# Optimization experiments

Hardware: AMD Instinct MI355X
Metric: run time of the kernel (lower is better)

## Reference

```python
import jax, jax.numpy as jnp
import numpy as np

IN_DIM, HID, MEM, OUT = 512, 1024, 1024, 512
BATCH = 4096
HIST = 5  # hist_steps hard-coded in MMU.__init__

_LINEARS = [("inpgate", IN_DIM, HID), ("rec_inpgate", OUT, HID), ("mem_inpgate", MEM, HID),
            ("inp", IN_DIM, HID), ("rec_inp", OUT, HID),
            ("readgate", IN_DIM, MEM), ("rec_readgate", OUT, MEM), ("mem_readgate", MEM, MEM),
            ("decoder", HID, MEM),
            ("writegate", IN_DIM, MEM), ("rec_writegate", OUT, MEM), ("mem_writegate", MEM, MEM),
            ("encoder", MEM, HID)]


def setup_inputs() -> dict:
    key = jax.random.key(0)
    ks = iter(jax.random.split(key, 2 * len(_LINEARS) + 4))
    d = {"input": jax.random.normal(next(ks), (IN_DIM, BATCH), jnp.float32)}
    for name, fin, fout in _LINEARS:
        bound = 1.0 / np.sqrt(fin)  # torch nn.Linear default init range
        d["W_" + name] = jax.random.uniform(next(ks), (fout, fin), jnp.float32, -bound, bound)
        d["b_" + name] = jax.random.uniform(next(ks), (fout,), jnp.float32, -bound, bound)
    d["w_hid_out"] = jax.random.uniform(next(ks), (OUT, MEM), jnp.float32)  # torch.rand
    return d


def reference(input, W_inpgate, b_inpgate, W_rec_inpgate, b_rec_inpgate,
              W_mem_inpgate, b_mem_inpgate, W_inp, b_inp, W_rec_inp, b_rec_inp,
              W_readgate, b_readgate, W_rec_readgate, b_rec_readgate,
              W_mem_readgate, b_mem_readgate, W_decoder, b_decoder,
              W_writegate, b_writegate, W_rec_writegate, b_rec_writegate,
              W_mem_writegate, b_mem_writegate, W_encoder, b_encoder, w_hid_out):
    B = input.shape[1]
    lin = lambda x, W, b: x @ W.T + b
    # fresh module: history is zeros except last slot = current input (transposed to [B, in])
    xs = jnp.concatenate([jnp.zeros((HIST - 1, B, IN_DIM), input.dtype), input.T[None]], axis=0)

    def step(carry, x):
        out, mem = carry  # [B, OUT], [B, MEM]
        block_inp = jax.nn.sigmoid(lin(x, W_inp, b_inp) + lin(out, W_rec_inp, b_rec_inp))
        inp_gate = jax.nn.sigmoid(lin(x, W_inpgate, b_inpgate) + lin(mem, W_mem_inpgate, b_mem_inpgate)
                                  + lin(out, W_rec_inpgate, b_rec_inpgate))
        read_gate = jax.nn.sigmoid(lin(x, W_readgate, b_readgate) + lin(mem, W_mem_readgate, b_mem_readgate)
                                   + lin(out, W_rec_readgate, b_rec_readgate))
        decoded_mem = lin(read_gate * mem, W_decoder, b_decoder)
        hidden = decoded_mem + block_inp * inp_gate  # [B, HID] (HID == MEM)
        write_gate = jax.nn.sigmoid(lin(x, W_writegate, b_writegate) + lin(mem, W_mem_writegate, b_mem_writegate)
                                    + lin(out, W_rec_writegate, b_rec_writegate))
        encoded = jnp.tanh(lin(hidden, W_encoder, b_encoder))
        mem = (1.0 - write_gate) * mem + write_gate * encoded
        out = hidden @ w_hid_out.T  # w_hid_out.mm(hidden.T).T
        return (out, mem), None

    init = (jnp.zeros((B, OUT), input.dtype), jnp.zeros((B, MEM), input.dtype))
    (out, _mem), _ = jax.lax.scan(step, init, xs)
    return out
```

## Files before the change

kernel.cpp:

```cpp
#include <hip/hip_runtime.h>
#include <hip/hip_bf16.h>
#include <math.h>

typedef __hip_bfloat16 bf16;
typedef __attribute__((ext_vector_type(8))) short s16x8;
typedef __attribute__((ext_vector_type(4))) float f32x4;

__device__ __forceinline__ float fsig(float x) {
  return __builtin_amdgcn_rcpf(1.0f + __expf(-x));
}
__device__ __forceinline__ float ftanh(float x) { return 2.0f * fsig(2.0f * x) - 1.0f; }
__device__ __forceinline__ float dot4(float4 a, float4 b) {
  return a.x * b.x + a.y * b.y + a.z * b.z + a.w * b.w;
}
__device__ __forceinline__ float wred(float s) {
#pragma unroll
  for (int off = 32; off > 0; off >>= 1) s += __shfl_down(s, off, 64);
  return s;
}

__global__ void setup(const float* __restrict__ W_inp, const float* __restrict__ W_ig,
                      const float* __restrict__ W_rg, const float* __restrict__ W_ho,
                      const float* __restrict__ W_dec, const float* __restrict__ W_enc,
                      const float* __restrict__ input,
                      const float* __restrict__ b_inp, const float* __restrict__ b_rinp,
                      const float* __restrict__ b_ig, const float* __restrict__ b_mig,
                      const float* __restrict__ b_rig, const float* __restrict__ b_wg,
                      const float* __restrict__ b_mwg, const float* __restrict__ b_rwg,
                      const float* __restrict__ b_dec, const float* __restrict__ b_enc,
                      bf16* __restrict__ Wcat,
                      bf16* __restrict__ WhoB, bf16* __restrict__ Wcat2, bf16* __restrict__ Wdt,
                      bf16* __restrict__ WencB, bf16* __restrict__ Xb,
                      float* __restrict__ out_s, float* __restrict__ mem_s,
                      float* __restrict__ vout, float* __restrict__ Web) {
  __shared__ float t[32][33];
  const int id = blockIdx.x, tid = threadIdx.x;
  if (id < 12288) {
    const int i = id * 256 + tid;
    if (i < 524288) {
      Wcat[i] = __float2bfloat16(W_inp[i]);
    } else if (i < 1048576) {
      Wcat[i] = __float2bfloat16(W_ig[i - 524288]);
    } else if (i < 1572864) {
      Wcat[i] = __float2bfloat16(W_rg[i - 1048576]);
    } else if (i < 2097152) {
      const int k = i - 1572864;
      const bf16 vv = __float2bfloat16(W_ho[k]);
      WhoB[k] = vv;
      Wcat2[(size_t)(k >> 10) * 2048 + (k & 1023)] = vv;
    } else {
      const int k = i - 2097152;
      WencB[k] = __float2bfloat16(W_enc[k]);
    }
  } else if (id < 14336) {
    const int b = id - 12288;
    const int i0 = (b >> 7) * 32, b0 = (b & 127) * 32;
    const int tx = tid & 31, ty = tid >> 5;
#pragma unroll
    for (int r = ty; r < 32; r += 8) t[r][tx] = input[(size_t)(i0 + r) * 4096 + b0 + tx];
    __syncthreads();
#pragma unroll
    for (int r = ty; r < 32; r += 8)
      Xb[(size_t)(b0 + r) * 512 + i0 + tx] = __float2bfloat16(t[tx][r]);
  } else if (id < 15360) {
    const int b = id - 14336;
    const int j0 = (b >> 5) * 32, k0 = (b & 31) * 32;
    const int tx = tid & 31, ty = tid >> 5;
#pragma unroll
    for (int r = ty; r < 32; r += 8) t[r][tx] = W_dec[(size_t)(j0 + r) * 1024 + k0 + tx];
    __syncthreads();
#pragma unroll
    for (int r = ty; r < 32; r += 8)
      Wdt[(size_t)(k0 + r) * 1024 + j0 + tx] = __float2bfloat16(t[tx][r]);
  } else if (id < 16896) {
    const int o = id - 15360;
    const float* row = (o < 512) ? (W_ho + (size_t)o * 1024) : (W_enc + (size_t)(o - 512) * 1024);
    const float4 a = *(const float4*)(row + tid * 4);
    const float4 b = *(const float4*)(b_dec + tid * 4);
    float s = wred(dot4(a, b));
    if ((tid & 63) == 0) t[0][tid >> 6] = s;
    __syncthreads();
    if (tid == 0) {
      const float d = t[0][0] + t[0][1] + t[0][2] + t[0][3];
      if (o < 512) vout[o] = d;
      else Web[o - 512] = d;
    }
  } else {
    const int id2 = id - 16896;
    const float4 bd = *(const float4*)(b_dec + tid * 4);
    const float4 v1 = *(const float4*)(b_inp + tid * 4);
    const float4 v2 = *(const float4*)(b_rinp + tid * 4);
    const float4 v3 = *(const float4*)(b_ig + tid * 4);
    const float4 v4 = *(const float4*)(b_mig + tid * 4);
    const float4 v5 = *(const float4*)(b_rig + tid * 4);
    float4 hv;
    hv.x = bd.x + fsig(v1.x + v2.x) * fsig(v3.x + v4.x + v5.x);
    hv.y = bd.y + fsig(v1.y + v2.y) * fsig(v3.y + v4.y + v5.y);
    hv.z = bd.z + fsig(v1.z + v2.z) * fsig(v3.z + v4.z + v5.z);
    hv.w = bd.w + fsig(v1.w + v2.w) * fsig(v3.w + v4.w + v5.w);
    const float* row =
        (id2 < 1024) ? (W_enc + (size_t)id2 * 1024) : (W_ho + (size_t)(id2 - 1024) * 1024);
    float s = wred(dot4(*(const float4*)(row + tid * 4), hv));
    if ((tid & 63) == 0) t[0][tid >> 6] = s;
    __syncthreads();
    if (tid == 0) {
      const float d = t[0][0] + t[0][1] + t[0][2] + t[0][3];
      if (id2 < 1024) {
        const float wg = fsig(b_wg[id2] + b_mwg[id2] + b_rwg[id2]);
        mem_s[id2] = wg * ftanh(b_enc[id2] + d);
      } else {
        out_s[id2 - 1024] = d;
      }
    }
  }
}

__global__ __launch_bounds__(256) void gates_pe(
    const float* __restrict__ Wri, const float* __restrict__ Wmig,
    const float* __restrict__ Wrig, const float* __restrict__ Wmrg,
    const float* __restrict__ Wrrg, const float* __restrict__ Wmwg,
    const float* __restrict__ Wrwg, const float* __restrict__ b_inp,
    const float* __restrict__ b_rinp, const float* __restrict__ b_ig,
    const float* __restrict__ b_mig, const float* __restrict__ b_rig,
    const float* __restrict__ b_rg, const float* __restrict__ b_mrg,
    const float* __restrict__ b_rrg, const float* __restrict__ b_wg,
    const float* __restrict__ b_mwg, const float* __restrict__ b_rwg,
    const float* __restrict__ out_s, const float* __restrict__ mem_s,
    float* __restrict__ rgm, float* __restrict__ h0v, float* __restrict__ wgv,
    const bf16* __restrict__ WhoB, const bf16* __restrict__ WencB,
    const bf16* __restrict__ Wdt, float* __restrict__ P, float* __restrict__ E,
    int pe_blocks) {
  __shared__ char smem[16384];
  const int tid = threadIdx.x;
  if ((int)blockIdx.x >= pe_blocks) {
    float(*red)[4] = (float(*)[4])smem;
    const int j = blockIdx.x - pe_blocks, lane = tid & 63, wave = tid >> 6;
    const float4 z = make_float4(0.f, 0.f, 0.f, 0.f);
    const float4 o4 = (tid < 128) ? *(const float4*)(out_s + tid * 4) : z;
    const float4 m4 = *(const float4*)(mem_s + tid * 4);
    float p[7];
    p[0] = dot4((tid < 128) ? *(const float4*)(Wri + (size_t)j * 512 + tid * 4) : z, o4);
    p[1] = dot4(*(const float4*)(Wmig + (size_t)j * 1024 + tid * 4), m4);
    p[2] = dot4((tid < 128) ? *(const float4*)(Wrig + (size_t)j * 512 + tid * 4) : z, o4);
    p[3] = dot4(*(const float4*)(Wmrg + (size_t)j * 1024 + tid * 4), m4);
    p[4] = dot4((tid < 128) ? *(const float4*)(Wrrg + (size_t)j * 512 + tid * 4) : z, o4);
    p[5] = dot4(*(const float4*)(Wmwg + (size_t)j * 1024 + tid * 4), m4);
    p[6] = dot4((tid < 128) ? *(const float4*)(Wrwg + (size_t)j * 512 + tid * 4) : z, o4);
#pragma unroll
    for (int d = 0; d < 7; ++d) {
      float s = wred(p[d]);
      if (lane == 0) red[d][wave] = s;
    }
    __syncthreads();
    if (tid == 0) {
      float D[7];
#pragma unroll
      for (int d = 0; d < 7; ++d) D[d] = red[d][0] + red[d][1] + red[d][2] + red[d][3];
      const float abi = b_inp[j] + b_rinp[j] + D[0];
      const float aig = b_ig[j] + b_mig[j] + b_rig[j] + D[1] + D[2];
      const float arg = b_rg[j] + b_mrg[j] + b_rrg[j] + D[3] + D[4];
      const float awg = b_wg[j] + b_mwg[j] + b_rwg[j] + D[5] + D[6];
      rgm[j] = fsig(arg) * mem_s[j];
      h0v[j] = fsig(abi) * fsig(aig);
      wgv[j] = fsig(awg);
    }
    return;
  }
  const int bi = blockIdx.x;
  const bf16* Ag;
  float* Cg;
  int m0, n0, kt0;
  if (bi < 256) {
    Ag = WhoB; Cg = P;
    m0 = ((bi >> 4) & 7) * 64; n0 = (bi & 15) * 64; kt0 = (bi >> 7) * 512;
  } else {
    const int b2 = bi - 256;
    Ag = WencB; Cg = E;
    m0 = ((b2 >> 4) & 15) * 64; n0 = (b2 & 15) * 64; kt0 = (b2 >> 8) * 512;
  }
  const int wave = tid >> 6, lane = tid & 63;
  const int wm = wave >> 1, wn = wave & 1;
  f32x4 acc[2][2] = {};
  for (int kt = kt0; kt < kt0 + 512; kt += 64) {
    __syncthreads();
#pragma unroll
    for (int i = 0; i < 2; ++i) {
      const int ci = i * 256 + tid;
      const int row = ci >> 3, ck = (ci & 7) ^ (row & 7);
      const bf16* g = Ag + (size_t)(m0 + row) * 1024 + kt + ck * 8;
      const unsigned lofs = (unsigned)__builtin_amdgcn_readfirstlane((i * 256 + wave * 64) * 16);
      __builtin_amdgcn_global_load_lds(
          (const __attribute__((address_space(1))) void*)g,
          (__attribute__((address_space(3))) void*)(smem + lofs), 16, 0, 0);
    }
#pragma unroll
    for (int i = 0; i < 2; ++i) {
      const int ci = i * 256 + tid;
      const int row = ci >> 3, ck = (ci & 7) ^ (row & 7);
      const bf16* g = Wdt + (size_t)(n0 + row) * 1024 + kt + ck * 8;
      const unsigned lofs =
          (unsigned)__builtin_amdgcn_readfirstlane(8192 + (i * 256 + wave * 64) * 16);
      __builtin_amdgcn_global_load_lds(
          (const __attribute__((address_space(1))) void*)g,
          (__attribute__((address_space(3))) void*)(smem + lofs), 16, 0, 0);
    }
    __syncthreads();
#pragma unroll
    for (int ks = 0; ks < 2; ++ks) {
      const int ckk = ks * 4 + (lane >> 4);
      s16x8 af[2];
#pragma unroll
      for (int i = 0; i < 2; ++i) {
        const int R = wm * 32 + i * 16 + (lane & 15);
        af[i] = *(const s16x8*)(smem + (R * 8 + (ckk ^ (R & 7))) * 16);
      }
#pragma unroll
      for (int j = 0; j < 2; ++j) {
        const int R = wn * 32 + j * 16 + (lane & 15);
        const s16x8 bfr = *(const s16x8*)(smem + 8192 + (R * 8 + (ckk ^ (R & 7))) * 16);
#pragma unroll
        for (int i = 0; i < 2; ++i)
          acc[i][j] = __builtin_amdgcn_mfma_f32_16x16x32_bf16(af[i], bfr, acc[i][j], 0, 0, 0);
      }
    }
  }
  const int mb = (lane >> 4) * 4, nb = lane & 15;
#pragma unroll
  for (int i = 0; i < 2; ++i) {
#pragma unroll
    for (int j = 0; j < 2; ++j) {
      const int col = n0 + wn * 32 + j * 16 + nb;
#pragma unroll
      for (int r = 0; r < 4; ++r) {
        const int rowg = m0 + wm * 32 + i * 16 + mb + r;
        atomicAdd(Cg + (size_t)rowg * 1024 + col, acc[i][j][r]);
      }
    }
  }
}

__global__ void step_fuse(const float* __restrict__ E, const float* __restrict__ Wenc,
                          const float* __restrict__ P, const float* __restrict__ Who,
                          const float* __restrict__ b_enc, const float* __restrict__ Web,
                          const float* __restrict__ vout, const float* __restrict__ rgm,
                          const float* __restrict__ h0v, const float* __restrict__ wgv,
                          float* __restrict__ mem_s, float* __restrict__ out_s) {
  __shared__ float red[4];
  const int id = blockIdx.x, tid = threadIdx.x;
  const float4 r4 = *(const float4*)(rgm + tid * 4);
  const float4 h4 = *(const float4*)(h0v + tid * 4);
  const float* Ar = (id < 1024) ? (E + (size_t)id * 1024) : (P + (size_t)(id - 1024) * 1024);
  const float* Br = (id < 1024) ? (Wenc + (size_t)id * 1024) : (Who + (size_t)(id - 1024) * 1024);
  const float s1 = dot4(*(const float4*)(Ar + tid * 4), r4);
  const float s2 = dot4(*(const float4*)(Br + tid * 4), h4);
  const float s = wred(s1 + s2);
  if ((tid & 63) == 0) red[tid >> 6] = s;
  __syncthreads();
  if (tid == 0) {
    const float d = red[0] + red[1] + red[2] + red[3];
    if (id < 1024) {
      const float wg = wgv[id];
      mem_s[id] = (1.0f - wg) * mem_s[id] + wg * ftanh(b_enc[id] + Web[id] + d);
    } else {
      out_s[id - 1024] = vout[id - 1024] + d;
    }
  }
}

__global__ void final_consts(const float* __restrict__ Wri, const float* __restrict__ Wmig,
                             const float* __restrict__ Wrig, const float* __restrict__ Wmrg,
                             const float* __restrict__ Wrrg, const float* __restrict__ b_inp,
                             const float* __restrict__ b_rinp, const float* __restrict__ b_ig,
                             const float* __restrict__ b_mig, const float* __restrict__ b_rig,
                             const float* __restrict__ b_rg, const float* __restrict__ b_mrg,
                             const float* __restrict__ b_rrg, const float* __restrict__ out_s,
                             const float* __restrict__ mem_s, const float* __restrict__ P,
                             float* __restrict__ ccat, bf16* __restrict__ Wcat2) {
  __shared__ float red[5][4];
  const int id = blockIdx.x, tid = threadIdx.x, lane = tid & 63, wave = tid >> 6;
  if (id < 1024) {
    const float4 z = make_float4(0.f, 0.f, 0.f, 0.f);
    const float4 o4 = (tid < 128) ? *(const float4*)(out_s + tid * 4) : z;
    const float4 m4 = *(const float4*)(mem_s + tid * 4);
    float p[5];
    p[0] = dot4((tid < 128) ? *(const float4*)(Wri + (size_t)id * 512 + tid * 4) : z, o4);
    p[1] = dot4(*(const float4*)(Wmig + (size_t)id * 1024 + tid * 4), m4);
    p[2] = dot4((tid < 128) ? *(const float4*)(Wrig + (size_t)id * 512 + tid * 4) : z, o4);
    p[3] = dot4(*(const float4*)(Wmrg + (size_t)id * 1024 + tid * 4), m4);
    p[4] = dot4((tid < 128) ? *(const float4*)(Wrrg + (size_t)id * 512 + tid * 4) : z, o4);
#pragma unroll
    for (int d = 0; d < 5; ++d) {
      float s = wred(p[d]);
      if (lane == 0) red[d][wave] = s;
    }
    __syncthreads();
    if (tid == 0) {
      float D[5];
#pragma unroll
      for (int d = 0; d < 5; ++d) D[d] = red[d][0] + red[d][1] + red[d][2] + red[d][3];
      ccat[id] = b_inp[id] + b_rinp[id] + D[0];
      ccat[1024 + id] = b_ig[id] + b_mig[id] + b_rig[id] + D[1] + D[2];
      ccat[2048 + id] = b_rg[id] + b_mrg[id] + b_rrg[id] + D[3] + D[4];
    }
  } else {
    const int idx = (id - 1024) * 256 + tid;
    const int q = idx >> 10, k = idx & 1023;
    Wcat2[(size_t)q * 2048 + 1024 + k] = __float2bfloat16(P[idx] * mem_s[k]);
  }
}

__global__ __launch_bounds__(256, 4) void gemm_gates(const bf16* __restrict__ A,
                                                     const bf16* __restrict__ Wcat,
                                                     const float* __restrict__ ccat,
                                                     bf16* __restrict__ Hcat) {
  __shared__ char smem[32768];
  const int tid = threadIdx.x, wave = tid >> 6, lane = tid & 63;
  const int wm = wave >> 1, wn = wave & 1;
  const int m0 = blockIdx.y * 64, n0 = blockIdx.x * 64;
  f32x4 acc[3][2][2] = {};

  for (int kt = 0; kt < 512; kt += 64) {
    __syncthreads();
#pragma unroll
    for (int i = 0; i < 2; ++i) {
      const int ci = i * 256 + tid;
      const int row = ci >> 3, ck = (ci & 7) ^ (row & 7);
      const bf16* g = A + (size_t)(m0 + row) * 512 + kt + ck * 8;
      const unsigned lofs = (unsigned)__builtin_amdgcn_readfirstlane((i * 256 + wave * 64) * 16);
      __builtin_amdgcn_global_load_lds(
          (const __attribute__((address_space(1))) void*)g,
          (__attribute__((address_space(3))) void*)(smem + lofs), 16, 0, 0);
    }
#pragma unroll
    for (int gI = 0; gI < 3; ++gI) {
      const bf16* Bp = Wcat + gI * 524288;
#pragma unroll
      for (int i = 0; i < 2; ++i) {
        const int ci = i * 256 + tid;
        const int row = ci >> 3, ck = (ci & 7) ^ (row & 7);
        const bf16* g = Bp + (size_t)(n0 + row) * 512 + kt + ck * 8;
        const unsigned lofs = (unsigned)__builtin_amdgcn_readfirstlane(
            8192 + gI * 8192 + (i * 256 + wave * 64) * 16);
        __builtin_amdgcn_global_load_lds(
            (const __attribute__((address_space(1))) void*)g,
            (__attribute__((address_space(3))) void*)(smem + lofs), 16, 0, 0);
      }
    }
    __syncthreads();

#pragma unroll
    for (int ks = 0; ks < 2; ++ks) {
      const int ckk = ks * 4 + (lane >> 4);
      s16x8 af[2];
#pragma unroll
      for (int i = 0; i < 2; ++i) {
        const int R = wm * 32 + i * 16 + (lane & 15);
        af[i] = *(const s16x8*)(smem + (R * 8 + (ckk ^ (R & 7))) * 16);
      }
#pragma unroll
      for (int gI = 0; gI < 3; ++gI) {
#pragma unroll
        for (int j = 0; j < 2; ++j) {
          const int R = wn * 32 + j * 16 + (lane & 15);
          const s16x8 bfr =
              *(const s16x8*)(smem + 8192 + gI * 8192 + (R * 8 + (ckk ^ (R & 7))) * 16);
#pragma unroll
          for (int i = 0; i < 2; ++i)
            acc[gI][i][j] =
                __builtin_amdgcn_mfma_f32_16x16x32_bf16(af[i], bfr, acc[gI][i][j], 0, 0, 0);
        }
      }
    }
  }

  __syncthreads();
  bf16* sm = (bf16*)smem;
  bf16* sr = (bf16*)smem + 5120;
  const int mb = (lane >> 4) * 4, nb = lane & 15;
#pragma unroll
  for (int i = 0; i < 2; ++i) {
#pragma unroll
    for (int j = 0; j < 2; ++j) {
      const int colL = wn * 32 + j * 16 + nb;
      const int jg = n0 + colL;
      const float c0 = ccat[jg], c1 = ccat[1024 + jg], c2 = ccat[2048 + jg];
#pragma unroll
      for (int r = 0; r < 4; ++r) {
        const int rowL = wm * 32 + i * 16 + mb + r;
        const float h = fsig(acc[0][i][j][r] + c0) * fsig(acc[1][i][j][r] + c1);
        const float rg = fsig(acc[2][i][j][r] + c2);
        sm[rowL * 80 + colL] = __float2bfloat16(h);
        sr[rowL * 80 + colL] = __float2bfloat16(rg);
      }
    }
  }
  __syncthreads();
#pragma unroll
  for (int pp = 0; pp < 2; ++pp) {
    const int c = pp * 256 + tid;
    const int row = c >> 3, cc = c & 7;
    const s16x8 v0 = *(const s16x8*)(sm + row * 80 + cc * 8);
    const s16x8 v1 = *(const s16x8*)(sr + row * 80 + cc * 8);
    *(s16x8*)(Hcat + (size_t)(m0 + row) * 2048 + n0 + cc * 8) = v0;
    *(s16x8*)(Hcat + (size_t)(m0 + row) * 2048 + 1024 + n0 + cc * 8) = v1;
  }
}

__global__ __launch_bounds__(256, 4) void gemm_out(const bf16* __restrict__ A,
                                                   const bf16* __restrict__ Bp,
                                                   const float* __restrict__ vout,
                                                   float* __restrict__ outF) {
  __shared__ char smem[16384];
  const int tid = threadIdx.x, wave = tid >> 6, lane = tid & 63;
  const int wm = wave >> 1, wn = wave & 1;
  const int m0 = blockIdx.y * 64, n0 = blockIdx.x * 64;
  f32x4 acc[2][2] = {};

  for (int kt = 0; kt < 2048; kt += 64) {
    __syncthreads();
#pragma unroll
    for (int i = 0; i < 2; ++i) {
      const int ci = i * 256 + tid;
      const int row = ci >> 3, ck = (ci & 7) ^ (row & 7);
      const bf16* g = A + (size_t)(m0 + row) * 2048 + kt + ck * 8;
      const unsigned lofs = (unsigned)__builtin_amdgcn_readfirstlane((i * 256 + wave * 64) * 16);
      __builtin_amdgcn_global_load_lds(
          (const __attribute__((address_space(1))) void*)g,
          (__attribute__((address_space(3))) void*)(smem + lofs), 16, 0, 0);
    }
#pragma unroll
    for (int i = 0; i < 2; ++i) {
      const int ci = i * 256 + tid;
      const int row = ci >> 3, ck = (ci & 7) ^ (row & 7);
      const bf16* g = Bp + (size_t)(n0 + row) * 2048 + kt + ck * 8;
      const unsigned lofs =
          (unsigned)__builtin_amdgcn_readfirstlane(8192 + (i * 256 + wave * 64) * 16);
      __builtin_amdgcn_global_load_lds(
          (const __attribute__((address_space(1))) void*)g,
          (__attribute__((address_space(3))) void*)(smem + lofs), 16, 0, 0);
    }
    __syncthreads();

#pragma unroll
    for (int ks = 0; ks < 2; ++ks) {
      const int ckk = ks * 4 + (lane >> 4);
      s16x8 af[2];
#pragma unroll
      for (int i = 0; i < 2; ++i) {
        const int R = wm * 32 + i * 16 + (lane & 15);
        af[i] = *(const s16x8*)(smem + (R * 8 + (ckk ^ (R & 7))) * 16);
      }
#pragma unroll
      for (int j = 0; j < 2; ++j) {
        const int R = wn * 32 + j * 16 + (lane & 15);
        const s16x8 bfr = *(const s16x8*)(smem + 8192 + (R * 8 + (ckk ^ (R & 7))) * 16);
#pragma unroll
        for (int i = 0; i < 2; ++i)
          acc[i][j] = __builtin_amdgcn_mfma_f32_16x16x32_bf16(af[i], bfr, acc[i][j], 0, 0, 0);
      }
    }
  }

  const int mb = (lane >> 4) * 4, nb = lane & 15;
#pragma unroll
  for (int i = 0; i < 2; ++i) {
#pragma unroll
    for (int j = 0; j < 2; ++j) {
      const int col = n0 + wn * 32 + j * 16 + nb;
#pragma unroll
      for (int r = 0; r < 4; ++r) {
        const int rowg = m0 + wm * 32 + i * 16 + mb + r;
        outF[(size_t)rowg * 512 + col] = acc[i][j][r] + vout[col];
      }
    }
  }
}

extern "C" void kernel_launch(void* const* d_in, const int* in_sizes, int n_in, void* d_out,
                              int out_size, void* d_ws, size_t ws_size, hipStream_t stream) {
  const float* input  = (const float*)d_in[0];
  const float* W_ig   = (const float*)d_in[1];  const float* b_ig   = (const float*)d_in[2];
  const float* W_rig  = (const float*)d_in[3];  const float* b_rig  = (const float*)d_in[4];
  const float* W_mig  = (const float*)d_in[5];  const float* b_mig  = (const float*)d_in[6];
  const float* W_inp  = (const float*)d_in[7];  const float* b_inp  = (const float*)d_in[8];
  const float* W_rinp = (const float*)d_in[9];  const float* b_rinp = (const float*)d_in[10];
  const float* W_rg   = (const float*)d_in[11]; const float* b_rg   = (const float*)d_in[12];
  const float* W_rrg  = (const float*)d_in[13]; const float* b_rrg  = (const float*)d_in[14];
  const float* W_mrg  = (const float*)d_in[15]; const float* b_mrg  = (const float*)d_in[16];
  const float* W_dec  = (const float*)d_in[17]; const float* b_dec  = (const float*)d_in[18];
  const float* W_wg   = (const float*)d_in[19]; const float* b_wg   = (const float*)d_in[20];
  const float* W_rwg  = (const float*)d_in[21]; const float* b_rwg  = (const float*)d_in[22];
  const float* W_mwg  = (const float*)d_in[23]; const float* b_mwg  = (const float*)d_in[24];
  const float* W_enc  = (const float*)d_in[25]; const float* b_enc  = (const float*)d_in[26];
  const float* W_ho   = (const float*)d_in[27];
  (void)W_wg;

  char* ws = (char*)d_ws;
  float* out_s = (float*)(ws + 0);
  float* mem_s = (float*)(ws + 4096);
  float* rgm   = (float*)(ws + 8192);
  float* h0v   = (float*)(ws + 12288);
  float* wgv   = (float*)(ws + 16384);
  float* ccat  = (float*)(ws + 24576);
  float* vout  = (float*)(ws + 40960);
  float* Web   = (float*)(ws + 45056);
  float* P     = (float*)(ws + 65536);
  bf16* Xb     = (bf16*)(ws + 2162688);
  bf16* Wcat   = (bf16*)(ws + 6356992);
  bf16* WhoB   = (bf16*)(ws + 9502720);
  bf16* Wcat2  = (bf16*)(ws + 10551296);
  bf16* Wdt    = (bf16*)(ws + 12648448);
  bf16* Hcat   = (bf16*)(ws + 14745600);
  float* E     = (float*)(ws + 31522816);
  bf16* WencB  = (bf16*)(ws + 35717120);

  setup<<<18432, 256, 0, stream>>>(W_inp, W_ig, W_rg, W_ho, W_dec, W_enc, input, b_inp, b_rinp,
                                   b_ig, b_mig, b_rig, b_wg, b_mwg, b_rwg, b_dec, b_enc, Wcat,
                                   WhoB, Wcat2, Wdt, WencB, Xb, out_s, mem_s, vout, Web);

  for (int s = 0; s < 3; ++s) {
    const int pe = (s == 0) ? 768 : 0;
    gates_pe<<<1024 + pe, 256, 0, stream>>>(W_rinp, W_mig, W_rig, W_mrg, W_rrg, W_mwg, W_rwg,
                                            b_inp, b_rinp, b_ig, b_mig, b_rig, b_rg, b_mrg,
                                            b_rrg, b_wg, b_mwg, b_rwg, out_s, mem_s, rgm, h0v,
                                            wgv, WhoB, WencB, Wdt, P, E, pe);
    step_fuse<<<1536, 256, 0, stream>>>(E, W_enc, P, W_ho, b_enc, Web, vout, rgm, h0v, wgv,
                                        mem_s, out_s);
  }

  final_consts<<<3072, 256, 0, stream>>>(W_rinp, W_mig, W_rig, W_mrg, W_rrg, b_inp, b_rinp, b_ig,
                                         b_mig, b_rig, b_rg, b_mrg, b_rrg, out_s, mem_s, P, ccat,
                                         Wcat2);

  gemm_gates<<<dim3(16, 64), 256, 0, stream>>>(Xb, Wcat, ccat, Hcat);

  gemm_out<<<dim3(8, 64), 256, 0, stream>>>(Hcat, Wcat2, vout, (float*)d_out);
}
```

Before: 227.7 us.

## Double-buffer GEMM LDS staging, drop split-K atomics, store P/E products in bf16

The precompute GEMM in gates_pe no longer splits K in two with fp32 atomicAdd. Each block now runs the full K=1024 and writes bf16 results directly, so there are half as many blocks. Both that GEMM and gemm_out now double-buffer their LDS tiles (32 KB), prefetching the next k-slice while MFMAs run on the current one. step_fuse and final_consts read the bf16 P/E products and the bf16 weight copies instead of fp32, which halves their read traffic. The costs are less parallelism in the step-0 GEMM, twice the shared memory per block (which may lower occupancy), and extra rounding error from bf16 intermediates.

```diff
diff --git a/kernel.cpp b/kernel.cpp
--- a/kernel.cpp
+++ b/kernel.cpp
@@ -17,6 +17,12 @@
 #pragma unroll
   for (int off = 32; off > 0; off >>= 1) s += __shfl_down(s, off, 64);
   return s;
+}
+__device__ __forceinline__ float b2f(unsigned short u) {
+  return __uint_as_float((unsigned)u << 16);
+}
+__device__ __forceinline__ float4 b2f4(ushort4 u) {
+  return make_float4(b2f(u.x), b2f(u.y), b2f(u.z), b2f(u.w));
 }
 
 __global__ void setup(const float* __restrict__ W_inp, const float* __restrict__ W_ig,
@@ -128,9 +134,9 @@
     const float* __restrict__ out_s, const float* __restrict__ mem_s,
     float* __restrict__ rgm, float* __restrict__ h0v, float* __restrict__ wgv,
     const bf16* __restrict__ WhoB, const bf16* __restrict__ WencB,
-    const bf16* __restrict__ Wdt, float* __restrict__ P, float* __restrict__ E,
+    const bf16* __restrict__ Wdt, bf16* __restrict__ Pb, bf16* __restrict__ Eb,
     int pe_blocks) {
-  __shared__ char smem[16384];
+  __shared__ char smem[32768];
   const int tid = threadIdx.x;
   if ((int)blockIdx.x >= pe_blocks) {
     float(*red)[4] = (float(*)[4])smem;
@@ -168,27 +174,28 @@
   }
   const int bi = blockIdx.x;
   const bf16* Ag;
-  float* Cg;
-  int m0, n0, kt0;
-  if (bi < 256) {
-    Ag = WhoB; Cg = P;
-    m0 = ((bi >> 4) & 7) * 64; n0 = (bi & 15) * 64; kt0 = (bi >> 7) * 512;
+  bf16* Cg;
+  int m0, n0;
+  if (bi < 128) {
+    Ag = WhoB; Cg = Pb;
+    m0 = (bi >> 4) * 64; n0 = (bi & 15) * 64;
   } else {
-    const int b2 = bi - 256;
-    Ag = WencB; Cg = E;
-    m0 = ((b2 >> 4) & 15) * 64; n0 = (b2 & 15) * 64; kt0 = (b2 >> 8) * 512;
+    const int b2 = bi - 128;
+    Ag = WencB; Cg = Eb;
+    m0 = (b2 >> 4) * 64; n0 = (b2 & 15) * 64;
   }
   const int wave = tid >> 6, lane = tid & 63;
   const int wm = wave >> 1, wn = wave & 1;
   f32x4 acc[2][2] = {};
-  for (int kt = kt0; kt < kt0 + 512; kt += 64) {
-    __syncthreads();
+
+  auto STAGE = [&](int kt, unsigned bofs) {
 #pragma unroll
     for (int i = 0; i < 2; ++i) {
       const int ci = i * 256 + tid;
       const int row = ci >> 3, ck = (ci & 7) ^ (row & 7);
       const bf16* g = Ag + (size_t)(m0 + row) * 1024 + kt + ck * 8;
-      const unsigned lofs = (unsigned)__builtin_amdgcn_readfirstlane((i * 256 + wave * 64) * 16);
+      const unsigned lofs =
+          (unsigned)__builtin_amdgcn_readfirstlane(bofs + (i * 256 + wave * 64) * 16);
       __builtin_amdgcn_global_load_lds(
           (const __attribute__((address_space(1))) void*)g,
           (__attribute__((address_space(3))) void*)(smem + lofs), 16, 0, 0);
@@ -199,30 +206,39 @@
       const int row = ci >> 3, ck = (ci & 7) ^ (row & 7);
       const bf16* g = Wdt + (size_t)(n0 + row) * 1024 + kt + ck * 8;
       const unsigned lofs =
-          (unsigned)__builtin_amdgcn_readfirstlane(8192 + (i * 256 + wave * 64) * 16);
+          (unsigned)__builtin_amdgcn_readfirstlane(bofs + 8192 + (i * 256 + wave * 64) * 16);
       __builtin_amdgcn_global_load_lds(
           (const __attribute__((address_space(1))) void*)g,
           (__attribute__((address_space(3))) void*)(smem + lofs), 16, 0, 0);
     }
-    __syncthreads();
+  };
+
+  STAGE(0, 0);
+  __syncthreads();
+  unsigned cur = 0;
+  for (int kt = 0; kt < 1024; kt += 64) {
+    if (kt + 64 < 1024) STAGE(kt + 64, (cur ^ 1u) * 16384u);
 #pragma unroll
     for (int ks = 0; ks < 2; ++ks) {
       const int ckk = ks * 4 + (lane >> 4);
+      const unsigned cofs = cur * 16384u;
       s16x8 af[2];
 #pragma unroll
       for (int i = 0; i < 2; ++i) {
         const int R = wm * 32 + i * 16 + (lane & 15);
-        af[i] = *(const s16x8*)(smem + (R * 8 + (ckk ^ (R & 7))) * 16);
+        af[i] = *(const s16x8*)(smem + cofs + (R * 8 + (ckk ^ (R & 7))) * 16);
       }
 #pragma unroll
       for (int j = 0; j < 2; ++j) {
         const int R = wn * 32 + j * 16 + (lane & 15);
-        const s16x8 bfr = *(const s16x8*)(smem + 8192 + (R * 8 + (ckk ^ (R & 7))) * 16);
+        const s16x8 bfr = *(const s16x8*)(smem + cofs + 8192 + (R * 8 + (ckk ^ (R & 7))) * 16);
 #pragma unroll
         for (int i = 0; i < 2; ++i)
           acc[i][j] = __builtin_amdgcn_mfma_f32_16x16x32_bf16(af[i], bfr, acc[i][j], 0, 0, 0);
       }
     }
+    __syncthreads();
+    cur ^= 1u;
   }
   const int mb = (lane >> 4) * 4, nb = lane & 15;
 #pragma unroll
@@ -233,14 +249,14 @@
 #pragma unroll
       for (int r = 0; r < 4; ++r) {
         const int rowg = m0 + wm * 32 + i * 16 + mb + r;
-        atomicAdd(Cg + (size_t)rowg * 1024 + col, acc[i][j][r]);
-      }
-    }
-  }
-}
-
-__global__ void step_fuse(const float* __restrict__ E, const float* __restrict__ Wenc,
-                          const float* __restrict__ P, const float* __restrict__ Who,
+        Cg[(size_t)rowg * 1024 + col] = __float2bfloat16(acc[i][j][r]);
+      }
+    }
+  }
+}
+
+__global__ void step_fuse(const bf16* __restrict__ Eb, const bf16* __restrict__ WencB,
+                          const bf16* __restrict__ Pb, const bf16* __restrict__ WhoB,
                           const float* __restrict__ b_enc, const float* __restrict__ Web,
                           const float* __restrict__ vout, const float* __restrict__ rgm,
                           const float* __restrict__ h0v, const float* __restrict__ wgv,
@@ -249,11 +265,12 @@
   const int id = blockIdx.x, tid = threadIdx.x;
   const float4 r4 = *(const float4*)(rgm + tid * 4);
   const float4 h4 = *(const float4*)(h0v + tid * 4);
-  const float* Ar = (id < 1024) ? (E + (size_t)id * 1024) : (P + (size_t)(id - 1024) * 1024);
-  const float* Br = (id < 1024) ? (Wenc + (size_t)id * 1024) : (Who + (size_t)(id - 1024) * 1024);
-  const float s1 = dot4(*(const float4*)(Ar + tid * 4), r4);
-  const float s2 = dot4(*(const float4*)(Br + tid * 4), h4);
-  const float s = wred(s1 + s2);
+  const bf16* Ar = (id < 1024) ? (Eb + (size_t)id * 1024) : (Pb + (size_t)(id - 1024) * 1024);
+  const bf16* Br =
+      (id < 1024) ? (WencB + (size_t)id * 1024) : (WhoB + (size_t)(id - 1024) * 1024);
+  const float4 a4 = b2f4(*(const ushort4*)(Ar + tid * 4));
+  const float4 b4 = b2f4(*(const ushort4*)(Br + tid * 4));
+  const float s = wred(dot4(a4, r4) + dot4(b4, h4));
   if ((tid & 63) == 0) red[tid >> 6] = s;
   __syncthreads();
   if (tid == 0) {
@@ -274,7 +291,7 @@
                              const float* __restrict__ b_mig, const float* __restrict__ b_rig,
                              const float* __restrict__ b_rg, const float* __restrict__ b_mrg,
                              const float* __restrict__ b_rrg, const float* __restrict__ out_s,
-                             const float* __restrict__ mem_s, const float* __restrict__ P,
+                             const float* __restrict__ mem_s, const bf16* __restrict__ Pb,
                              float* __restrict__ ccat, bf16* __restrict__ Wcat2) {
   __shared__ float red[5][4];
   const int id = blockIdx.x, tid = threadIdx.x, lane = tid & 63, wave = tid >> 6;
@@ -304,8 +321,9 @@
     }
   } else {
     const int idx = (id - 1024) * 256 + tid;
-    const int q = idx >> 10, k = idx & 1023;
-    Wcat2[(size_t)q * 2048 + 1024 + k] = __float2bfloat16(P[idx] * mem_s[k]);
+    const int k = idx & 1023;
+    const float pv = b2f(((const unsigned short*)Pb)[idx]);
+    Wcat2[(size_t)(idx >> 10) * 2048 + 1024 + k] = __float2bfloat16(pv * mem_s[k]);
   }
 }
 
@@ -410,20 +428,20 @@
                                                    const bf16* __restrict__ Bp,
                                                    const float* __restrict__ vout,
                                                    float* __restrict__ outF) {
-  __shared__ char smem[16384];
+  __shared__ char smem[32768];
   const int tid = threadIdx.x, wave = tid >> 6, lane = tid & 63;
   const int wm = wave >> 1, wn = wave & 1;
   const int m0 = blockIdx.y * 64, n0 = blockIdx.x * 64;
   f32x4 acc[2][2] = {};
 
-  for (int kt = 0; kt < 2048; kt += 64) {
-    __syncthreads();
+  auto STAGE = [&](int kt, unsigned bofs) {
 #pragma unroll
     for (int i = 0; i < 2; ++i) {
       const int ci = i * 256 + tid;
       const int row = ci >> 3, ck = (ci & 7) ^ (row & 7);
       const bf16* g = A + (size_t)(m0 + row) * 2048 + kt + ck * 8;
-      const unsigned lofs = (unsigned)__builtin_amdgcn_readfirstlane((i * 256 + wave * 64) * 16);
+      const unsigned lofs =
+          (unsigned)__builtin_amdgcn_readfirstlane(bofs + (i * 256 + wave * 64) * 16);
       __builtin_amdgcn_global_load_lds(
           (const __attribute__((address_space(1))) void*)g,
           (__attribute__((address_space(3))) void*)(smem + lofs), 16, 0, 0);
@@ -434,31 +452,39 @@
       const int row = ci >> 3, ck = (ci & 7) ^ (row & 7);
       const bf16* g = Bp + (size_t)(n0 + row) * 2048 + kt + ck * 8;
       const unsigned lofs =
-          (unsigned)__builtin_amdgcn_readfirstlane(8192 + (i * 256 + wave * 64) * 16);
+          (unsigned)__builtin_amdgcn_readfirstlane(bofs + 8192 + (i * 256 + wave * 64) * 16);
       __builtin_amdgcn_global_load_lds(
           (const __attribute__((address_space(1))) void*)g,
           (__attribute__((address_space(3))) void*)(smem + lofs), 16, 0, 0);
     }
-    __syncthreads();
-
+  };
+
+  STAGE(0, 0);
+  __syncthreads();
+  unsigned cur = 0;
+  for (int kt = 0; kt < 2048; kt += 64) {
+    if (kt + 64 < 2048) STAGE(kt + 64, (cur ^ 1u) * 16384u);
 #pragma unroll
     for (int ks = 0; ks < 2; ++ks) {
       const int ckk = ks * 4 + (lane >> 4);
+      const unsigned cofs = cur * 16384u;
       s16x8 af[2];
 #pragma unroll
       for (int i = 0; i < 2; ++i) {
         const int R = wm * 32 + i * 16 + (lane & 15);
-        af[i] = *(const s16x8*)(smem + (R * 8 + (ckk ^ (R & 7))) * 16);
+        af[i] = *(const s16x8*)(smem + cofs + (R * 8 + (ckk ^ (R & 7))) * 16);
       }
 #pragma unroll
       for (int j = 0; j < 2; ++j) {
         const int R = wn * 32 + j * 16 + (lane & 15);
-        const s16x8 bfr = *(const s16x8*)(smem + 8192 + (R * 8 + (ckk ^ (R & 7))) * 16);
+        const s16x8 bfr = *(const s16x8*)(smem + cofs + 8192 + (R * 8 + (ckk ^ (R & 7))) * 16);
 #pragma unroll
         for (int i = 0; i < 2; ++i)
           acc[i][j] = __builtin_amdgcn_mfma_f32_16x16x32_bf16(af[i], bfr, acc[i][j], 0, 0, 0);
       }
     }
+    __syncthreads();
+    cur ^= 1u;
   }
 
   const int mb = (lane >> 4) * 4, nb = lane & 15;
@@ -504,14 +530,14 @@
   float* ccat  = (float*)(ws + 24576);
   float* vout  = (float*)(ws + 40960);
   float* Web   = (float*)(ws + 45056);
-  float* P     = (float*)(ws + 65536);
+  bf16* Pb     = (bf16*)(ws + 65536);
   bf16* Xb     = (bf16*)(ws + 2162688);
   bf16* Wcat   = (bf16*)(ws + 6356992);
   bf16* WhoB   = (bf16*)(ws + 9502720);
   bf16* Wcat2  = (bf16*)(ws + 10551296);
   bf16* Wdt    = (bf16*)(ws + 12648448);
   bf16* Hcat   = (bf16*)(ws + 14745600);
-  float* E     = (float*)(ws + 31522816);
+  bf16* Eb     = (bf16*)(ws + 31522816);
   bf16* WencB  = (bf16*)(ws + 35717120);
 
   setup<<<18432, 256, 0, stream>>>(W_inp, W_ig, W_rg, W_ho, W_dec, W_enc, input, b_inp, b_rinp,
@@ -519,18 +545,18 @@
                                    WhoB, Wcat2, Wdt, WencB, Xb, out_s, mem_s, vout, Web);
 
   for (int s = 0; s < 3; ++s) {
-    const int pe = (s == 0) ? 768 : 0;
+    const int pe = (s == 0) ? 384 : 0;
     gates_pe<<<1024 + pe, 256, 0, stream>>>(W_rinp, W_mig, W_rig, W_mrg, W_rrg, W_mwg, W_rwg,
                                             b_inp, b_rinp, b_ig, b_mig, b_rig, b_rg, b_mrg,
                                             b_rrg, b_wg, b_mwg, b_rwg, out_s, mem_s, rgm, h0v,
-                                            wgv, WhoB, WencB, Wdt, P, E, pe);
-    step_fuse<<<1536, 256, 0, stream>>>(E, W_enc, P, W_ho, b_enc, Web, vout, rgm, h0v, wgv,
+                                            wgv, WhoB, WencB, Wdt, Pb, Eb, pe);
+    step_fuse<<<1536, 256, 0, stream>>>(Eb, WencB, Pb, WhoB, b_enc, Web, vout, rgm, h0v, wgv,
                                         mem_s, out_s);
   }
 
   final_consts<<<3072, 256, 0, stream>>>(W_rinp, W_mig, W_rig, W_mrg, W_rrg, b_inp, b_rinp, b_ig,
-                                         b_mig, b_rig, b_rg, b_mrg, b_rrg, out_s, mem_s, P, ccat,
-                                         Wcat2);
+                                         b_mig, b_rig, b_rg, b_mrg, b_rrg, out_s, mem_s, Pb,
+                                         ccat, Wcat2);
 
   gemm_gates<<<dim3(16, 64), 256, 0, stream>>>(Xb, Wcat, ccat, Hcat);
 
```

After: 215.4 us. 1.06x faster.
